# Optimization experiments

Hardware: AMD Instinct MI355X
Metric: run time of the kernel (lower is better)

Reference implementation:

```python
import jax, jax.numpy as jnp
import numpy as np
from functools import partial

RES = 512          # image resolution (source uses 1024; scaled for CPU baseline)
BLOB_COUNT = 2048  # number of Gaussian blobs (source uses 4096)
CHUNK = 64         # blobs processed per scan step to bound intermediates


def setup_inputs() -> dict:
    key = jax.random.key(0)
    k_pos, k_scale, k_rot, k_col = jax.random.split(key, 4)
    pos = jax.random.uniform(k_pos, (BLOB_COUNT, 2))                      # blob centers in [0,1]^2
    scale = 0.005 + 0.05 * jax.random.uniform(k_scale, (BLOB_COUNT, 2))   # per-axis std dev
    rot = 2.0 * jnp.pi * jax.random.uniform(k_rot, (BLOB_COUNT, 1))       # rotation angle
    color = jax.random.uniform(k_col, (BLOB_COUNT, 3))                    # rgb intensity
    blobs = jnp.concatenate([pos, scale, rot, color], axis=-1).astype(jnp.float32)  # [N, 8]
    return {"blobs": blobs}


def _splat(blobs):
    H = W = RES
    # pixel centers in normalized [0,1] coords
    ys = (jnp.arange(H, dtype=jnp.float32) + 0.5) / H
    xs = (jnp.arange(W, dtype=jnp.float32) + 0.5) / W
    py, px = jnp.meshgrid(ys, xs, indexing="ij")  # [H, W]

    def body(img, chunk):  # chunk: [CHUNK, 8]
        pos = chunk[:, 0:2]
        sx = chunk[:, 2][:, None, None]
        sy = chunk[:, 3][:, None, None]
        rot = chunk[:, 4]
        color = chunk[:, 5:8]
        c = jnp.cos(rot)[:, None, None]
        s = jnp.sin(rot)[:, None, None]
        dx = px[None] - pos[:, 0][:, None, None]   # [C, H, W]
        dy = py[None] - pos[:, 1][:, None, None]
        xr = c * dx + s * dy                        # rotate into blob frame
        yr = -s * dx + c * dy
        g = jnp.exp(-0.5 * ((xr / sx) ** 2 + (yr / sy) ** 2))  # [C, H, W]
        img = img + jnp.einsum("chw,ck->hwk", g, color)
        return img, None

    img0 = jnp.zeros((H, W, 3), dtype=blobs.dtype)
    chunks = blobs.reshape(BLOB_COUNT // CHUNK, CHUNK, 8)
    img, _ = jax.lax.scan(jax.checkpoint(body), img0, chunks)
    return img


@jax.jit
def reference(blobs):
    return _splat(blobs)
```

## Files before the change

kernel.cpp:

```cpp
#include <hip/hip_runtime.h>
#include <math.h>

#define RES     512
#define NBLOB   2048
#define TILE_W  32
#define TILE_H  16
#define ROWS_T  8
#define TX_N    (RES / TILE_W)
#define TY_N    (RES / TILE_H)
#define CHUNK_B 256
#define NCHUNK  (NBLOB / CHUNK_B)
#define K_CONST   0.84932184f
#define SQRT_CULL 3.4641016f
#define HALFDIAG  0.0336327f

__device__ __forceinline__ float fast_exp2(float x) {
#if __has_builtin(__builtin_amdgcn_exp2f)
    return __builtin_amdgcn_exp2f(x);
#else
    return exp2f(x);
#endif
}

__global__ __launch_bounds__(256) void splat_kernel(const float* __restrict__ blobs,
                                                    float* __restrict__ out) {
    __shared__ int sh_cnt[NCHUNK];
    __shared__ float4 sh_p0[2][CHUNK_B];
    __shared__ float4 sh_p1[2][CHUNK_B];
    __shared__ float  sh_p2[2][CHUNK_B];

    const int tid = threadIdx.x;
    const int lane = tid & 63;
    const int tx = blockIdx.x;
    const int ty = blockIdx.y;

    if (tid < NCHUNK) sh_cnt[tid] = 0;

    const int x  = tx * TILE_W + (tid & 31);
    const int y0 = ty * TILE_H + (tid >> 5);
    const float fx  = (x + 0.5f) * (1.0f / RES);
    const float fy0 = (y0 + 0.5f) * (1.0f / RES);
    const float DY  = (float)ROWS_T * (1.0f / RES);

    const float cxT = (tx * TILE_W + 16.0f) * (1.0f / RES);
    const float cyT = (ty * TILE_H + 8.0f) * (1.0f / RES);

    float ar0 = 0.f, ag0 = 0.f, ab0 = 0.f;
    float ar1 = 0.f, ag1 = 0.f, ab1 = 0.f;

    float4 rb0 = *(const float4*)(blobs + (size_t)tid * 8);
    float4 rb1 = *(const float4*)(blobs + (size_t)tid * 8 + 4);

    __syncthreads();

    for (int c = 0; c < NCHUNK; ++c) {
        const float sx = rb0.z, sy = rb0.w;
        float sn, cn;
        __sincosf(rb1.x, &sn, &cn);
        const float isx = K_CONST / sx;
        const float isy = K_CONST / sy;
        const float ma =  cn * isx;
        const float mb =  sn * isx;
        const float md = -sn * isy;
        const float me =  cn * isy;
        const float opn = K_CONST / fminf(sx, sy);
        const float rt  = SQRT_CULL + opn * HALFDIAG;
        const float dxc = cxT - rb0.x;
        const float dyc = cyT - rb0.y;
        const float uc = ma * dxc + mb * dyc;
        const float vc = md * dxc + me * dyc;
        const bool hit = fmaf(uc, uc, vc * vc) <= rt * rt;

        const unsigned long long mask = __ballot(hit);
        const int total = __popcll(mask);
        int base = 0;
        if (lane == 0 && total > 0) base = atomicAdd(&sh_cnt[c], total);
        base = __builtin_amdgcn_readfirstlane(base);
        const int buf = c & 1;
        if (hit) {
            const int pos = base + __popcll(mask & ((1ull << lane) - 1ull));
            sh_p0[buf][pos] = make_float4(rb0.x, rb0.y, ma, mb);
            sh_p1[buf][pos] = make_float4(md, me, rb1.y, rb1.z);
            sh_p2[buf][pos] = rb1.w;
        }

        const int jn = (c + 1 < NCHUNK ? c + 1 : c) * CHUNK_B + tid;
        const float4 nb0 = *(const float4*)(blobs + (size_t)jn * 8);
        const float4 nb1 = *(const float4*)(blobs + (size_t)jn * 8 + 4);

        __syncthreads();

        const int n = sh_cnt[c];
        #pragma unroll 4
        for (int k = 0; k < n; ++k) {
            const float4 p0 = sh_p0[buf][k];
            const float4 p1 = sh_p1[buf][k];
            const float  cb = sh_p2[buf][k];
            const float dx = fx - p0.x;
            const float dy = fy0 - p0.y;
            float u = p0.z * dx + p0.w * dy;
            float v = p1.x * dx + p1.y * dy;

            const float g0 = fast_exp2(-fmaf(u, u, v * v));
            u += p0.w * DY; v += p1.y * DY;
            const float g1 = fast_exp2(-fmaf(u, u, v * v));

            ar0 += g0 * p1.z;  ag0 += g0 * p1.w;  ab0 += g0 * cb;
            ar1 += g1 * p1.z;  ag1 += g1 * p1.w;  ab1 += g1 * cb;
        }

        rb0 = nb0;
        rb1 = nb1;
    }

    const int b0i = (y0 * RES + x) * 3;
    out[b0i + 0] = ar0;  out[b0i + 1] = ag0;  out[b0i + 2] = ab0;
    const int b1i = ((y0 + ROWS_T) * RES + x) * 3;
    out[b1i + 0] = ar1;  out[b1i + 1] = ag1;  out[b1i + 2] = ab1;
}

extern "C" void kernel_launch(void* const* d_in, const int* in_sizes, int n_in,
                              void* d_out, int out_size, void* d_ws, size_t ws_size,
                              hipStream_t stream) {
    const float* blobs = (const float*)d_in[0];
    float* out = (float*)d_out;
    (void)d_ws; (void)ws_size;

    hipLaunchKernelGGL(splat_kernel, dim3(TX_N, TY_N), dim3(256), 0, stream,
                       blobs, out);
}
```

Measured before the change: 73.52 us.

## Tighten tile culling with exact rect-ellipse test and pack blob params

Replaces the bounding-circle tile cull with an exact minimum of the blob's quadratic form over the tile rectangle. It takes the minimum over the four tile edges, plus an inside test for blob centres within the tile, and uses a lower threshold. This is meant to drop more blobs from each tile's list and shorten the inner loop. It also precomputes the affine offsets so the per-pixel projection becomes pure FMAs. Red and green are packed as half2, which cuts per-blob shared-memory entries from three arrays to two float4s. The cost is more per-blob setup work and reduced colour precision. The lower cutoff also slightly changes accuracy.

```diff
diff --git a/kernel.cpp b/kernel.cpp
--- a/kernel.cpp
+++ b/kernel.cpp
@@ -1,4 +1,5 @@
 #include <hip/hip_runtime.h>
+#include <hip/hip_fp16.h>
 #include <math.h>
 
 #define RES     512
@@ -10,9 +11,8 @@
 #define TY_N    (RES / TILE_H)
 #define CHUNK_B 256
 #define NCHUNK  (NBLOB / CHUNK_B)
-#define K_CONST   0.84932184f
-#define SQRT_CULL 3.4641016f
-#define HALFDIAG  0.0336327f
+#define K_CONST 0.84932184f
+#define CULL_Q  10.0f
 
 __device__ __forceinline__ float fast_exp2(float x) {
 #if __has_builtin(__builtin_amdgcn_exp2f)
@@ -27,7 +27,6 @@
     __shared__ int sh_cnt[NCHUNK];
     __shared__ float4 sh_p0[2][CHUNK_B];
     __shared__ float4 sh_p1[2][CHUNK_B];
-    __shared__ float  sh_p2[2][CHUNK_B];
 
     const int tid = threadIdx.x;
     const int lane = tid & 63;
@@ -42,8 +41,10 @@
     const float fy0 = (y0 + 0.5f) * (1.0f / RES);
     const float DY  = (float)ROWS_T * (1.0f / RES);
 
-    const float cxT = (tx * TILE_W + 16.0f) * (1.0f / RES);
-    const float cyT = (ty * TILE_H + 8.0f) * (1.0f / RES);
+    const float rx0 = (tx * TILE_W + 0.5f) * (1.0f / RES);
+    const float rx1 = (tx * TILE_W + (TILE_W - 0.5f)) * (1.0f / RES);
+    const float ry0 = (ty * TILE_H + 0.5f) * (1.0f / RES);
+    const float ry1 = (ty * TILE_H + (TILE_H - 0.5f)) * (1.0f / RES);
 
     float ar0 = 0.f, ag0 = 0.f, ab0 = 0.f;
     float ar1 = 0.f, ag1 = 0.f, ab1 = 0.f;
@@ -54,6 +55,7 @@
     __syncthreads();
 
     for (int c = 0; c < NCHUNK; ++c) {
+        const float px = rb0.x, py = rb0.y;
         const float sx = rb0.z, sy = rb0.w;
         float sn, cn;
         __sincosf(rb1.x, &sn, &cn);
@@ -63,13 +65,46 @@
         const float mb =  sn * isx;
         const float md = -sn * isy;
         const float me =  cn * isy;
-        const float opn = K_CONST / fminf(sx, sy);
-        const float rt  = SQRT_CULL + opn * HALFDIAG;
-        const float dxc = cxT - rb0.x;
-        const float dyc = cyT - rb0.y;
-        const float uc = ma * dxc + mb * dyc;
-        const float vc = md * dxc + me * dyc;
-        const bool hit = fmaf(uc, uc, vc * vc) <= rt * rt;
+
+        const float dlx = rx0 - px, dhx = rx1 - px;
+        const float dly = ry0 - py, dhy = ry1 - py;
+        const bool inside = (dlx <= 0.f) & (dhx >= 0.f) & (dly <= 0.f) & (dhy >= 0.f);
+
+        const float n1 = ma * ma + md * md;
+        const float n2 = mb * mb + me * me;
+        const float i1 = __frcp_rn(n1);
+        const float i2 = __frcp_rn(n2);
+
+        float qmin;
+        {
+            const float A = ma * dlx, B = md * dlx;
+            float t = -(mb * A + me * B) * i2;
+            t = fminf(fmaxf(t, dly), dhy);
+            const float w1 = fmaf(mb, t, A), w2 = fmaf(me, t, B);
+            qmin = fmaf(w1, w1, w2 * w2);
+        }
+        {
+            const float A = ma * dhx, B = md * dhx;
+            float t = -(mb * A + me * B) * i2;
+            t = fminf(fmaxf(t, dly), dhy);
+            const float w1 = fmaf(mb, t, A), w2 = fmaf(me, t, B);
+            qmin = fminf(qmin, fmaf(w1, w1, w2 * w2));
+        }
+        {
+            const float A = mb * dly, B = me * dly;
+            float s = -(ma * A + md * B) * i1;
+            s = fminf(fmaxf(s, dlx), dhx);
+            const float w1 = fmaf(ma, s, A), w2 = fmaf(md, s, B);
+            qmin = fminf(qmin, fmaf(w1, w1, w2 * w2));
+        }
+        {
+            const float A = mb * dhy, B = me * dhy;
+            float s = -(ma * A + md * B) * i1;
+            s = fminf(fmaxf(s, dlx), dhx);
+            const float w1 = fmaf(ma, s, A), w2 = fmaf(md, s, B);
+            qmin = fminf(qmin, fmaf(w1, w1, w2 * w2));
+        }
+        const bool hit = inside | (qmin <= CULL_Q);
 
         const unsigned long long mask = __ballot(hit);
         const int total = __popcll(mask);
@@ -79,9 +114,13 @@
         const int buf = c & 1;
         if (hit) {
             const int pos = base + __popcll(mask & ((1ull << lane) - 1ull));
-            sh_p0[buf][pos] = make_float4(rb0.x, rb0.y, ma, mb);
-            sh_p1[buf][pos] = make_float4(md, me, rb1.y, rb1.z);
-            sh_p2[buf][pos] = rb1.w;
+            const float cu = -(ma * px + mb * py);
+            const float cv = -(md * px + me * py);
+            __half2 h2 = __floats2half2_rn(rb1.y, rb1.z);
+            float crcg;
+            *reinterpret_cast<__half2*>(&crcg) = h2;
+            sh_p0[buf][pos] = make_float4(ma, mb, cu, crcg);
+            sh_p1[buf][pos] = make_float4(md, me, cv, rb1.w);
         }
 
         const int jn = (c + 1 < NCHUNK ? c + 1 : c) * CHUNK_B + tid;
@@ -95,18 +134,21 @@
         for (int k = 0; k < n; ++k) {
             const float4 p0 = sh_p0[buf][k];
             const float4 p1 = sh_p1[buf][k];
-            const float  cb = sh_p2[buf][k];
-            const float dx = fx - p0.x;
-            const float dy = fy0 - p0.y;
-            float u = p0.z * dx + p0.w * dy;
-            float v = p1.x * dx + p1.y * dy;
+            const __half2 h2 = *reinterpret_cast<const __half2*>(&p0.w);
+            const float cr = __half2float(h2.x);
+            const float cg = __half2float(h2.y);
+            const float cb = p1.w;
+
+            float u = fmaf(p0.x, fx, fmaf(p0.y, fy0, p0.z));
+            float v = fmaf(p1.x, fx, fmaf(p1.y, fy0, p1.z));
 
             const float g0 = fast_exp2(-fmaf(u, u, v * v));
-            u += p0.w * DY; v += p1.y * DY;
+            u = fmaf(p0.y, DY, u);
+            v = fmaf(p1.y, DY, v);
             const float g1 = fast_exp2(-fmaf(u, u, v * v));
 
-            ar0 += g0 * p1.z;  ag0 += g0 * p1.w;  ab0 += g0 * cb;
-            ar1 += g1 * p1.z;  ag1 += g1 * p1.w;  ab1 += g1 * cb;
+            ar0 += g0 * cr;  ag0 += g0 * cg;  ab0 += g0 * cb;
+            ar1 += g1 * cr;  ag1 += g1 * cg;  ab1 += g1 * cb;
         }
 
         rb0 = nb0;
```

Result: no change. 72.53 us (-1.3%).
